# Performance work log

Measured on AMD Instinct MI355X. Metric: run time of the kernel, lower is better.

The kernel has to match this reference:

```python
import jax, jax.numpy as jnp
import numpy as np

B, P, C, F = 16, 1000, 91, 1024      # images, proposals/img, classes (incl bg), box-head dim
H, W = 800, 800                      # image shape (all images same size)
SCORE_THRESH = 0.05
NMS_THRESH = 0.5
DETS = 100                           # detections_per_img
MIN_SIZE = 1e-2
BBOX_XFORM_CLIP = float(np.log(1000.0 / 16.0))
OFF = float(max(H, W) + 2)           # class offset unit for batched (class-aware) NMS


def setup_inputs() -> dict:
    key = jax.random.key(0)
    k1, k2, k3, k4 = jax.random.split(key, 4)
    box_features = jax.random.normal(k1, (B * P, F), jnp.float32)
    Wc = jax.random.normal(k2, (F, C), jnp.float32) * 0.02
    bc = jnp.zeros((C,), jnp.float32)
    Wb = jax.random.normal(k3, (F, C * 4), jnp.float32) * 0.02
    bb = jnp.zeros((C * 4,), jnp.float32)
    u = jax.random.uniform(k4, (B, P, 4), jnp.float32)
    x1 = u[..., 0] * (W * 0.8)
    y1 = u[..., 1] * (H * 0.8)
    x2 = x1 + 16.0 + u[..., 2] * (W * 0.2)
    y2 = y1 + 16.0 + u[..., 3] * (H * 0.2)
    proposals = jnp.stack([x1, y1, x2, y2], axis=-1)
    return dict(box_features=box_features, Wc=Wc, bc=bc, Wb=Wb, bb=bb,
                proposals=proposals)


def _decode_and_clip(regs, props):
    # regs: [N, C, 4] deltas; props: [N, 4] xyxy. bbox_reg_weights = (1,1,1,1).
    w = props[:, 2] - props[:, 0]
    h = props[:, 3] - props[:, 1]
    cx = props[:, 0] + 0.5 * w
    cy = props[:, 1] + 0.5 * h
    dx, dy = regs[..., 0], regs[..., 1]
    dw = jnp.minimum(regs[..., 2], BBOX_XFORM_CLIP)
    dh = jnp.minimum(regs[..., 3], BBOX_XFORM_CLIP)
    pcx = dx * w[:, None] + cx[:, None]
    pcy = dy * h[:, None] + cy[:, None]
    pw = jnp.exp(dw) * w[:, None]
    ph = jnp.exp(dh) * h[:, None]
    x1 = jnp.clip(pcx - 0.5 * pw, 0.0, float(W))
    y1 = jnp.clip(pcy - 0.5 * ph, 0.0, float(H))
    x2 = jnp.clip(pcx + 0.5 * pw, 0.0, float(W))
    y2 = jnp.clip(pcy + 0.5 * ph, 0.0, float(H))
    return jnp.stack([x1, y1, x2, y2], axis=-1)  # [N, C, 4]


def _iou_one_vs_all(box, boxes):
    ix1 = jnp.maximum(box[0], boxes[:, 0])
    iy1 = jnp.maximum(box[1], boxes[:, 1])
    ix2 = jnp.minimum(box[2], boxes[:, 2])
    iy2 = jnp.minimum(box[3], boxes[:, 3])
    inter = jnp.clip(ix2 - ix1, 0.0) * jnp.clip(iy2 - iy1, 0.0)
    a1 = (box[2] - box[0]) * (box[3] - box[1])
    a2 = (boxes[:, 2] - boxes[:, 0]) * (boxes[:, 3] - boxes[:, 1])
    return inter / (a1 + a2 - inter + 1e-9)


def _greedy_nms(boxes, scores):
    # boxes: [M,4] (class-offset), scores: [M] (-inf = filtered out).
    # Returns selected indices [DETS] and scores [DETS] (0 where no valid pick).
    def body(i, st):
        sc, sel, ss = st
        j = jnp.argmax(sc)
        s = sc[j]
        iou = _iou_one_vs_all(boxes[j], boxes)
        sc = jnp.where(iou > NMS_THRESH, -jnp.inf, sc)  # suppresses j itself too
        valid = s > 0.0
        sel = sel.at[i].set(jnp.where(valid, j.astype(jnp.int32), 0))
        ss = ss.at[i].set(jnp.where(valid, s, 0.0))
        return sc, sel, ss
    init = (scores, jnp.zeros((DETS,), jnp.int32), jnp.zeros((DETS,), jnp.float32))
    _, sel, ss = jax.lax.fori_loop(0, DETS, body, init)
    return sel, ss


def reference(box_features, Wc, bc, Wb, bb, proposals):
    # Box predictor (FastRCNNPredictor-style linear heads).
    class_logits = box_features @ Wc + bc                  # [B*P, C]
    box_regression = (box_features @ Wb + bb).reshape(-1, C, 4)
    # Decode per-class boxes against proposals, clip to image.
    pred = _decode_and_clip(box_regression, proposals.reshape(-1, 4))  # [B*P, C, 4]
    scores = jax.nn.softmax(class_logits, axis=-1)         # [B*P, C]
    # Drop background class 0; flatten (proposal, class) per image.
    M = P * (C - 1)
    boxes_all = pred[:, 1:, :].reshape(B, M, 4)
    scores_all = scores[:, 1:].reshape(B, M)
    labels_all = jnp.tile(jnp.arange(1, C, dtype=jnp.int32), P)  # [M]
    # Score threshold + remove tiny boxes (mask instead of dynamic filter).
    bw = boxes_all[..., 2] - boxes_all[..., 0]
    bh = boxes_all[..., 3] - boxes_all[..., 1]
    keep = (scores_all > SCORE_THRESH) & (bw >= MIN_SIZE) & (bh >= MIN_SIZE)
    scores_m = jnp.where(keep, scores_all, -jnp.inf)
    # Class-aware batched NMS via per-class coordinate offsets.
    boxes_off = boxes_all + (labels_all.astype(jnp.float32) * OFF)[None, :, None]
    sel, det_scores = jax.vmap(_greedy_nms)(boxes_off, scores_m)   # [B,DETS]
    det_boxes = jnp.take_along_axis(boxes_all, sel[..., None], axis=1)  # [B,DETS,4]
    det_labels = labels_all[sel]                                        # [B,DETS]
    valid = det_scores > 0.0
    det_boxes = det_boxes * valid[..., None]
    det_labels = jnp.where(valid, det_labels, 0)
    return det_boxes, det_scores, det_labels
```

## Files before the change

### kernel.cpp

```cpp
#include <hip/hip_runtime.h>
#include <hip/hip_bf16.h>
#include <math.h>

typedef unsigned long long ull;
typedef __attribute__((ext_vector_type(8))) short bf16x8;
typedef __attribute__((ext_vector_type(4))) float f32x4;

#define BB_ 16
#define PP_ 1000
#define CC_ 91
#define FF_ 1024
#define DETS_ 100
#define CAP_ 2048
#define CAND_MAX (BB_ * CAP_)
#define SURV_CAP 2048
#define CLS_CAP 256
#define BLK_CAND 720
#define IMG_W 800.0f
#define IMG_H 800.0f
#define OFF_ 802.0f
#define SCORE_TH 0.05f
#define PRE_TH 0.0494f
#define NMS_TH 0.5f
#define MIN_SZ 0.01f
#define BBOX_CLIP_D 4.135166556742356

__device__ __forceinline__ ushort bf16_hi(float v) {
    return (ushort)((__float_as_uint(v) + 0x8000u) >> 16);
}

__global__ __launch_bounds__(256) void prep_weights(
    const float* __restrict__ Wb, float* __restrict__ Wbt,
    const float* __restrict__ Wc, ushort* __restrict__ Wcth,
    ushort* __restrict__ Wctl)
{
    const int idx = blockIdx.x * 256 + threadIdx.x;
    if (idx < CC_ * 4 * FF_) {
        const int c = idx >> 12;
        const int j = (idx >> 10) & 3;
        const int k = idx & 1023;
        Wbt[idx] = (c < 1) ? 0.f : Wb[(size_t)k * (CC_ * 4) + 4 * c + j];
    }
    if (idx < 96 * FF_) {
        const int c = idx >> 10, k = idx & 1023;
        const float v = (c < CC_) ? Wc[(size_t)k * CC_ + c] : 0.f;
        const ushort h = bf16_hi(v);
        const float hf = __uint_as_float(((unsigned)h) << 16);
        Wcth[idx] = h;
        Wctl[idx] = bf16_hi(v - hf);
    }
}

__global__ __launch_bounds__(256) void prepass_mfma(
    const float* __restrict__ A, const ushort* __restrict__ Wcth,
    const ushort* __restrict__ Wctl, const float* __restrict__ bc,
    int* __restrict__ rowlist, int* __restrict__ nrowsp)
{
    __shared__ union __align__(16) SM {
        struct { ushort Ah[32][40]; ushort Al[32][40];
                 ushort Bh[96][40]; ushort Bl[96][40]; } t;
        float Ssc[32][97];
    } sm;

    const int tid = threadIdx.x;
    const int row0 = blockIdx.x * 32;
    const int lane = tid & 63;
    const int w = tid >> 6;
    const int rowOff = (w & 1) * 16;
    const int colOff = (w >> 1) * 48;

    const int arow = tid >> 3;
    const int ak4 = (tid & 7) * 4;
    const int bcol = tid >> 1;
    const int bkh = (tid & 1) * 16;

    f32x4 acc0 = {0.f, 0.f, 0.f, 0.f};
    f32x4 acc1 = {0.f, 0.f, 0.f, 0.f};
    f32x4 acc2 = {0.f, 0.f, 0.f, 0.f};

    float4 avP = *(const float4*)(A + (size_t)(row0 + arow) * FF_ + ak4);
    uint4 bhP0 = make_uint4(0,0,0,0), bhP1 = make_uint4(0,0,0,0);
    uint4 blP0 = make_uint4(0,0,0,0), blP1 = make_uint4(0,0,0,0);
    if (tid < 192) {
        const ushort* sh = Wcth + (size_t)bcol * FF_ + bkh;
        const ushort* sl = Wctl + (size_t)bcol * FF_ + bkh;
        bhP0 = *(const uint4*)(sh);  bhP1 = *(const uint4*)(sh + 8);
        blP0 = *(const uint4*)(sl);  blP1 = *(const uint4*)(sl + 8);
    }

    for (int k0 = 0; k0 < FF_; k0 += 32) {
        {
            float vv[4] = {avP.x, avP.y, avP.z, avP.w};
            ushort hh[4], ll[4];
#pragma unroll
            for (int j = 0; j < 4; ++j) {
                hh[j] = bf16_hi(vv[j]);
                const float hf = __uint_as_float(((unsigned)hh[j]) << 16);
                ll[j] = bf16_hi(vv[j] - hf);
            }
            *(uint2*)&sm.t.Ah[arow][ak4] = make_uint2(
                (unsigned)hh[0] | ((unsigned)hh[1] << 16),
                (unsigned)hh[2] | ((unsigned)hh[3] << 16));
            *(uint2*)&sm.t.Al[arow][ak4] = make_uint2(
                (unsigned)ll[0] | ((unsigned)ll[1] << 16),
                (unsigned)ll[2] | ((unsigned)ll[3] << 16));
        }
        if (tid < 192) {
            *(uint4*)&sm.t.Bh[bcol][bkh]     = bhP0;
            *(uint4*)&sm.t.Bh[bcol][bkh + 8] = bhP1;
            *(uint4*)&sm.t.Bl[bcol][bkh]     = blP0;
            *(uint4*)&sm.t.Bl[bcol][bkh + 8] = blP1;
        }

        const int kn = k0 + 32;
        if (kn < FF_) {
            avP = *(const float4*)(A + (size_t)(row0 + arow) * FF_ + kn + ak4);
            if (tid < 192) {
                const ushort* sh = Wcth + (size_t)bcol * FF_ + kn + bkh;
                const ushort* sl = Wctl + (size_t)bcol * FF_ + kn + bkh;
                bhP0 = *(const uint4*)(sh);  bhP1 = *(const uint4*)(sh + 8);
                blP0 = *(const uint4*)(sl);  blP1 = *(const uint4*)(sl + 8);
            }
        }
        __syncthreads();

        const int ar = rowOff + (lane & 15);
        const int ke = (lane >> 4) * 8;
        const bf16x8 aH = *(const bf16x8*)&sm.t.Ah[ar][ke];
        const bf16x8 aL = *(const bf16x8*)&sm.t.Al[ar][ke];
#pragma unroll
        for (int ct = 0; ct < 3; ++ct) {
            const int bc_ = colOff + ct * 16 + (lane & 15);
            const bf16x8 bH = *(const bf16x8*)&sm.t.Bh[bc_][ke];
            const bf16x8 bL = *(const bf16x8*)&sm.t.Bl[bc_][ke];
            f32x4* acc = (ct == 0) ? &acc0 : (ct == 1) ? &acc1 : &acc2;
            *acc = __builtin_amdgcn_mfma_f32_16x16x32_bf16(aH, bH, *acc, 0, 0, 0);
            *acc = __builtin_amdgcn_mfma_f32_16x16x32_bf16(aH, bL, *acc, 0, 0, 0);
            *acc = __builtin_amdgcn_mfma_f32_16x16x32_bf16(aL, bH, *acc, 0, 0, 0);
        }
        __syncthreads();
    }

    {
        const int r0 = rowOff + (lane >> 4) * 4;
        const int cb = colOff + (lane & 15);
#pragma unroll
        for (int reg = 0; reg < 4; ++reg) {
            const int row = r0 + reg;
            int c = cb;
            if (c < CC_) sm.Ssc[row][c] = acc0[reg] + bc[c];
            c = cb + 16;
            if (c < CC_) sm.Ssc[row][c] = acc1[reg] + bc[c];
            c = cb + 32;
            if (c < CC_) sm.Ssc[row][c] = acc2[reg] + bc[c];
        }
    }
    __syncthreads();

    if (tid < 32) {
        float m_all = sm.Ssc[tid][0];
        float m_fg = -INFINITY;
        for (int c = 1; c < CC_; ++c) {
            const float lv = sm.Ssc[tid][c];
            m_all = fmaxf(m_all, lv);
            m_fg = fmaxf(m_fg, lv);
        }
        float denom = 0.f;
        for (int c = 0; c < CC_; ++c) denom += expf(sm.Ssc[tid][c] - m_all);
        const float maxsc = expf(m_fg - m_all) / denom;
        if (maxsc > PRE_TH) {
            const int pos = atomicAdd(nrowsp, 1);
            rowlist[pos] = row0 + tid;
        }
    }
}

template<bool USE_T>
__global__ __launch_bounds__(512) void logits_fp64_rows(
    const float* __restrict__ A, const float* __restrict__ Wc,
    const float* __restrict__ bc,
    const float* __restrict__ Wb, const float* __restrict__ Wbt,
    const float* __restrict__ bb, const float* __restrict__ props,
    const int* __restrict__ rowlist, const int* __restrict__ nrowsp,
    float* __restrict__ cs, int* __restrict__ clab,
    int* __restrict__ corig, int* __restrict__ cpidx,
    int* __restrict__ cnt,
    float* __restrict__ cx1, float* __restrict__ cy1,
    float* __restrict__ cx2, float* __restrict__ cy2)
{
    const int nr = *nrowsp;
    const int row0 = blockIdx.x * 8;
    if (row0 >= nr) return;

    __shared__ union __align__(16) SM {
        struct { float Af[2][32][12]; float Bs[2][32][98]; } t;
        struct { int cp[BLK_CAND]; int cc[BLK_CAND]; int cg[BLK_CAND]; } d;
    } sm;
    __shared__ __align__(16) double dcomb[256][3];
    __shared__ float Ssc[8][97];
    __shared__ int ncand;

    const int tid = threadIdx.x;
    const int kg = tid >> 8;
    const int l = tid & 255;
    const int kbase = kg * 512;
    const int r = l >> 5;
    const int c0 = (l & 31) * 3;

    if (tid == 0) ncand = 0;

    const int aslot = l >> 3;
    const int akq = (l & 7) * 4;
    const float* Arow = nullptr;
    if (l < 64) {
        const int ridx = min(row0 + aslot, nr - 1);
        Arow = A + (size_t)rowlist[ridx] * FF_ + kbase;
    }
    const int bk = l >> 3;
    const int bn = (l & 7) * 12;

    double acc[3] = {0.0, 0.0, 0.0};

    float4 avP = make_float4(0.f, 0.f, 0.f, 0.f);
    if (l < 64) avP = *reinterpret_cast<const float4*>(Arow + akq);
    float bvP[12];
#pragma unroll
    for (int jj = 0; jj < 12; ++jj) {
        const int c = bn + jj;
        bvP[jj] = (c < CC_) ? Wc[(size_t)(kbase + bk) * CC_ + c] : 0.f;
    }

    for (int k0 = 0; k0 < 512; k0 += 32) {
        if (l < 64) {
            sm.t.Af[kg][akq + 0][aslot] = avP.x;
            sm.t.Af[kg][akq + 1][aslot] = avP.y;
            sm.t.Af[kg][akq + 2][aslot] = avP.z;
            sm.t.Af[kg][akq + 3][aslot] = avP.w;
        }
#pragma unroll
        for (int jj = 0; jj < 12; ++jj) sm.t.Bs[kg][bk][bn + jj] = bvP[jj];

        const int kn = k0 + 32;
        if (kn < 512) {
            if (l < 64)
                avP = *reinterpret_cast<const float4*>(Arow + kn + akq);
#pragma unroll
            for (int jj = 0; jj < 12; ++jj) {
                const int c = bn + jj;
                bvP[jj] = (c < CC_) ? Wc[(size_t)(kbase + kn + bk) * CC_ + c] : 0.f;
            }
        }
        __syncthreads();

#pragma unroll
        for (int k = 0; k < 32; ++k) {
            const double a0 = (double)sm.t.Af[kg][k][r];
            const double b0 = (double)sm.t.Bs[kg][k][c0 + 0];
            const double b1 = (double)sm.t.Bs[kg][k][c0 + 1];
            const double b2 = (double)sm.t.Bs[kg][k][c0 + 2];
            acc[0] += a0 * b0;
            acc[1] += a0 * b1;
            acc[2] += a0 * b2;
        }
        __syncthreads();
    }

    if (kg == 1) {
#pragma unroll
        for (int j = 0; j < 3; ++j) dcomb[l][j] = acc[j];
    }
    __syncthreads();
    if (kg == 0) {
#pragma unroll
        for (int j = 0; j < 3; ++j) {
            const int c = c0 + j;
            if (c < CC_) {
                const double v = acc[j] + dcomb[l][j];
                Ssc[r][c] = __fadd_rn((float)v, bc[c]);
            }
        }
    }
    __syncthreads();

    {
        const int w = tid >> 6;
        const int lane = tid & 63;
        if (w < 8 && row0 + w < nr) {
            const int p = rowlist[row0 + w];
            const int b = p / PP_;
            const int pi = p - b * PP_;

            const float l1 = Ssc[w][lane];
            const float l2 = (lane < CC_ - 64) ? Ssc[w][lane + 64] : -INFINITY;
            float m = fmaxf(l1, l2);
#pragma unroll
            for (int off = 32; off > 0; off >>= 1)
                m = fmaxf(m, __shfl_xor(m, off));

            double d = exp((double)l1 - (double)m);
            if (lane < CC_ - 64) d += exp((double)l2 - (double)m);
#pragma unroll
            for (int off = 1; off < 64; off <<= 1)
                d += __shfl_xor(d, off);

#pragma unroll
            for (int q = 0; q < 2; ++q) {
                const int c = lane + q * 64;
                if (c >= 1 && c < CC_) {
                    const double sd = exp((double)Ssc[w][c] - (double)m) / d;
                    const float score = (float)sd;
                    if (score > SCORE_TH) {
                        const int pos = atomicAdd(&cnt[b], 1);
                        if (pos < CAP_) {
                            const int g = b * CAP_ + pos;
                            cs[g] = score;
                            clab[g] = c;
                            corig[g] = pi * (CC_ - 1) + (c - 1);
                            cpidx[g] = p;
                            const int slot = atomicAdd(&ncand, 1);
                            if (slot < BLK_CAND) {
                                sm.d.cp[slot] = p;
                                sm.d.cc[slot] = c;
                                sm.d.cg[slot] = g;
                            }
                        }
                    }
                }
            }
        }
    }
    __syncthreads();

    {
        const int w = tid >> 6;
        const int lane = tid & 63;
        const int nc = min(ncand, BLK_CAND);
        for (int ci = w; ci < nc; ci += 8) {
            const int p = sm.d.cp[ci];
            const int c = sm.d.cc[ci];
            const int g = sm.d.cg[ci];

            const float* fr = A + (size_t)p * FF_;
            double a0 = 0.0, a1 = 0.0, a2 = 0.0, a3 = 0.0;
            if (USE_T) {
                const float* w0 = Wbt + (size_t)c * 4096;
                for (int k = lane; k < FF_; k += 64) {
                    const double f = (double)fr[k];
                    a0 += f * (double)w0[k];
                    a1 += f * (double)w0[1024 + k];
                    a2 += f * (double)w0[2048 + k];
                    a3 += f * (double)w0[3072 + k];
                }
            } else {
                const float* wb0 = Wb + 4 * c;
                for (int k = lane; k < FF_; k += 64) {
                    const double f = (double)fr[k];
                    const float4 wv = *reinterpret_cast<const float4*>(
                        wb0 + (size_t)k * (CC_ * 4));
                    a0 += f * (double)wv.x; a1 += f * (double)wv.y;
                    a2 += f * (double)wv.z; a3 += f * (double)wv.w;
                }
            }
#pragma unroll
            for (int off = 32; off > 0; off >>= 1) {
                a0 += __shfl_xor(a0, off);
                a1 += __shfl_xor(a1, off);
                a2 += __shfl_xor(a2, off);
                a3 += __shfl_xor(a3, off);
            }

            if (lane == 0) {
                const float dx = __fadd_rn((float)a0, bb[4 * c + 0]);
                const float dy = __fadd_rn((float)a1, bb[4 * c + 1]);
                const float clipf = (float)BBOX_CLIP_D;
                const float dw = fminf(__fadd_rn((float)a2, bb[4 * c + 2]), clipf);
                const float dh = fminf(__fadd_rn((float)a3, bb[4 * c + 3]), clipf);

                const float px1 = props[(size_t)p * 4 + 0];
                const float py1 = props[(size_t)p * 4 + 1];
                const float px2 = props[(size_t)p * 4 + 2];
                const float py2 = props[(size_t)p * 4 + 3];
                const float wq = __fsub_rn(px2, px1);
                const float hq = __fsub_rn(py2, py1);
                const float cxq = __fadd_rn(px1, __fmul_rn(0.5f, wq));
                const float cyq = __fadd_rn(py1, __fmul_rn(0.5f, hq));

                const float pcx = __fadd_rn(__fmul_rn(dx, wq), cxq);
                const float pcy = __fadd_rn(__fmul_rn(dy, hq), cyq);
                const float ew = (float)exp((double)dw);
                const float eh = (float)exp((double)dh);
                const float pw = __fmul_rn(ew, wq);
                const float ph = __fmul_rn(eh, hq);

                const float hw = __fmul_rn(0.5f, pw);
                const float hh = __fmul_rn(0.5f, ph);
                const float bx1 = fminf(fmaxf(__fsub_rn(pcx, hw), 0.f), IMG_W);
                const float by1 = fminf(fmaxf(__fsub_rn(pcy, hh), 0.f), IMG_H);
                const float bx2 = fminf(fmaxf(__fadd_rn(pcx, hw), 0.f), IMG_W);
                const float by2 = fminf(fmaxf(__fadd_rn(pcy, hh), 0.f), IMG_H);

                cx1[g] = bx1; cy1[g] = by1; cx2[g] = bx2; cy2[g] = by2;
                if (!(__fsub_rn(bx2, bx1) >= MIN_SZ && __fsub_rn(by2, by1) >= MIN_SZ)) {
                    cs[g] = -INFINITY;
                }
            }
        }
    }
}

__global__ __launch_bounds__(64) void nms_class(
    const float* __restrict__ c_x1, const float* __restrict__ c_y1,
    const float* __restrict__ c_x2, const float* __restrict__ c_y2,
    const float* __restrict__ c_s, const int* __restrict__ c_lab,
    const int* __restrict__ c_orig, const int* __restrict__ cnt,
    ull* __restrict__ skey, float* __restrict__ sx1v, float* __restrict__ sy1v,
    float* __restrict__ sx2v, float* __restrict__ sy2v,
    int* __restrict__ slabv, int* __restrict__ scnt)
{
    const int blk = blockIdx.x;
    const int b = blk / (CC_ - 1);
    const int c = 1 + (blk - b * (CC_ - 1));
    const int lane = threadIdx.x;

    __shared__ ull kk[CLS_CAP];
    __shared__ float x1s[CLS_CAP], y1s[CLS_CAP], x2s[CLS_CAP], y2s[CLS_CAP];

    const int n = min(cnt[b], CAP_);

    int mcnt = 0;
    for (int i0 = 0; i0 < n; i0 += 64) {
        const int i = i0 + lane;
        bool take = false;
        float s = 0.f; int so = 0; int g = 0;
        if (i < n) {
            g = b * CAP_ + i;
            if (c_lab[g] == c) {
                s = c_s[g];
                if (s > 0.f) { take = true; so = c_orig[g]; }
            }
        }
        const ull bal = __ballot(take);
        if (take) {
            const int pos = mcnt + __popcll(bal & ((1ull << lane) - 1ull));
            if (pos < CLS_CAP) {
                kk[pos] = ((ull)__float_as_uint(s) << 32) |
                          (unsigned int)(0x7FFFFFFF - so);
                x1s[pos] = c_x1[g]; y1s[pos] = c_y1[g];
                x2s[pos] = c_x2[g]; y2s[pos] = c_y2[g];
            }
        }
        mcnt += (int)__popcll(bal);
    }
    mcnt = min(mcnt, CLS_CAP);
    if (mcnt == 0) return;
    __syncthreads();

    while (true) {
        ull best = 0ull;
        for (int i = lane; i < mcnt; i += 64) best = (kk[i] > best) ? kk[i] : best;
#pragma unroll
        for (int off = 32; off > 0; off >>= 1) {
            const ull o = __shfl_xor(best, off);
            best = (o > best) ? o : best;
        }
        if (best == 0ull) break;

        int wsl = -1;
        for (int i = lane; i < mcnt; i += 64) if (kk[i] == best) wsl = i;
        const ull bal = __ballot(wsl >= 0);
        const int wlane = (int)__ffsll((long long)bal) - 1;
        wsl = __shfl(wsl, wlane);

        const float wx1 = x1s[wsl], wy1 = y1s[wsl];
        const float wx2 = x2s[wsl], wy2 = y2s[wsl];

        if (lane == 0) {
            const int sp = atomicAdd(&scnt[b], 1);
            if (sp < SURV_CAP) {
                const int sg = b * SURV_CAP + sp;
                skey[sg] = best;
                sx1v[sg] = wx1; sy1v[sg] = wy1;
                sx2v[sg] = wx2; sy2v[sg] = wy2;
                slabv[sg] = c;
            }
        }

        const float off = __fmul_rn((float)c, OFF_);
        const float ax1 = __fadd_rn(wx1, off), ay1 = __fadd_rn(wy1, off);
        const float ax2 = __fadd_rn(wx2, off), ay2 = __fadd_rn(wy2, off);
        const float a1 = __fmul_rn(__fsub_rn(ax2, ax1), __fsub_rn(ay2, ay1));
        for (int i = lane; i < mcnt; i += 64) {
            if (kk[i] == 0ull) continue;
            const float bx1 = __fadd_rn(x1s[i], off), by1 = __fadd_rn(y1s[i], off);
            const float bx2 = __fadd_rn(x2s[i], off), by2 = __fadd_rn(y2s[i], off);
            const float ix1 = fmaxf(ax1, bx1), iy1 = fmaxf(ay1, by1);
            const float ix2 = fminf(ax2, bx2), iy2 = fminf(ay2, by2);
            const float inter = __fmul_rn(fmaxf(__fsub_rn(ix2, ix1), 0.f),
                                          fmaxf(__fsub_rn(iy2, iy1), 0.f));
            const float a2 = __fmul_rn(__fsub_rn(bx2, bx1), __fsub_rn(by2, by1));
            const float den = __fadd_rn(__fsub_rn(__fadd_rn(a1, a2), inter), 1e-9f);
            const float iou = __fdiv_rn(inter, den);
            if (iou > NMS_TH) kk[i] = 0ull;
        }
        __syncthreads();
    }
}

__global__ __launch_bounds__(256) void nms_merge(
    const ull* __restrict__ skey, const float* __restrict__ sx1v,
    const float* __restrict__ sy1v, const float* __restrict__ sx2v,
    const float* __restrict__ sy2v, const int* __restrict__ slabv,
    const int* __restrict__ scnt, float* __restrict__ out)
{
    const int b = blockIdx.x;
    const int t = threadIdx.x;

    __shared__ ull k_[SURV_CAP];
    __shared__ int id_[SURV_CAP];

    const int m = min(scnt[b], SURV_CAP);
    int N2 = 128;
    while (N2 < m) N2 <<= 1;

    for (int i = t; i < N2; i += 256) {
        k_[i] = (i < m) ? skey[b * SURV_CAP + i] : 0ull;
        id_[i] = i;
    }
    __syncthreads();

    for (int ksz = 2; ksz <= N2; ksz <<= 1) {
        for (int j = ksz >> 1; j > 0; j >>= 1) {
            for (int i = t; i < N2; i += 256) {
                const int ixj = i ^ j;
                if (ixj > i) {
                    const ull a = k_[i], cc = k_[ixj];
                    const bool desc = ((i & ksz) == 0);
                    if (desc ? (a < cc) : (a > cc)) {
                        k_[i] = cc; k_[ixj] = a;
                        const int tmp = id_[i]; id_[i] = id_[ixj]; id_[ixj] = tmp;
                    }
                }
            }
            __syncthreads();
        }
    }

    const int boxes_base = 0;
    const int scores_base = BB_ * DETS_ * 4;
    const int labels_base = BB_ * DETS_ * 5;

    for (int r = t; r < DETS_; r += 256) {
        const ull key = (r < N2) ? k_[r] : 0ull;
        float* bo = out + boxes_base + (size_t)(b * DETS_ + r) * 4;
        if (key != 0ull) {
            const int sg = b * SURV_CAP + id_[r];
            bo[0] = sx1v[sg]; bo[1] = sy1v[sg];
            bo[2] = sx2v[sg]; bo[3] = sy2v[sg];
            out[scores_base + b * DETS_ + r] = __uint_as_float((unsigned)(key >> 32));
            out[labels_base + b * DETS_ + r] = (float)slabv[sg];
        } else {
            bo[0] = 0.f; bo[1] = 0.f; bo[2] = 0.f; bo[3] = 0.f;
            out[scores_base + b * DETS_ + r] = 0.f;
            out[labels_base + b * DETS_ + r] = 0.f;
        }
    }
}

extern "C" void kernel_launch(void* const* d_in, const int* in_sizes, int n_in,
                              void* d_out, int out_size, void* d_ws, size_t ws_size,
                              hipStream_t stream)
{
    const float* feat  = (const float*)d_in[0];
    const float* Wc    = (const float*)d_in[1];
    const float* bc    = (const float*)d_in[2];
    const float* Wb    = (const float*)d_in[3];
    const float* bb    = (const float*)d_in[4];
    const float* props = (const float*)d_in[5];
    for (int i = 0; i < n_in; ++i) {
        const float* q = (const float*)d_in[i];
        switch (in_sizes[i]) {
            case 16384000: feat  = q; break;
            case 93184:    Wc    = q; break;
            case 91:       bc    = q; break;
            case 372736:   Wb    = q; break;
            case 364:      bb    = q; break;
            case 64000:    props = q; break;
        }
    }
    float* out = (float*)d_out;

    char* ws = (char*)d_ws;
    int*   cnt    = (int*)ws;
    int*   scnt   = (int*)(ws + 64);
    int*   nrowsp = (int*)(ws + 128);
    float* cs    = (float*)(ws + 256);
    int*   clab  = (int*)(cs + CAND_MAX);
    int*   corig = clab + CAND_MAX;
    int*   cpidx = corig + CAND_MAX;
    float* cx1   = (float*)(cpidx + CAND_MAX);
    float* cy1   = cx1 + CAND_MAX;
    float* cx2   = cy1 + CAND_MAX;
    float* cy2   = cx2 + CAND_MAX;
    ull*   skey  = (ull*)(cy2 + CAND_MAX);
    float* sx1v  = (float*)(skey + (size_t)BB_ * SURV_CAP);
    float* sy1v  = sx1v + (size_t)BB_ * SURV_CAP;
    float* sx2v  = sy1v + (size_t)BB_ * SURV_CAP;
    float* sy2v  = sx2v + (size_t)BB_ * SURV_CAP;
    int*   slabv = (int*)(sy2v + (size_t)BB_ * SURV_CAP);
    int*   rowlist = slabv + (size_t)BB_ * SURV_CAP;
    ushort* Wcth = (ushort*)(rowlist + 16384);
    ushort* Wctl = Wcth + 96 * FF_;
    float* Wbt   = (float*)(Wctl + 96 * FF_);

    const size_t need = ((char*)(Wbt + CC_ * 4 * FF_)) - ws;
    const bool useT = (ws_size >= need);

    hipMemsetAsync(ws, 0, 256, stream);

    prep_weights<<<(CC_ * 4 * FF_ + 255) / 256, 256, 0, stream>>>(
        Wb, Wbt, Wc, Wcth, Wctl);

    prepass_mfma<<<BB_ * PP_ / 32, 256, 0, stream>>>(feat, Wcth, Wctl, bc,
        rowlist, nrowsp);

    if (useT)
        logits_fp64_rows<true><<<BB_ * PP_ / 8, 512, 0, stream>>>(
            feat, Wc, bc, Wb, Wbt, bb, props, rowlist, nrowsp,
            cs, clab, corig, cpidx, cnt, cx1, cy1, cx2, cy2);
    else
        logits_fp64_rows<false><<<BB_ * PP_ / 8, 512, 0, stream>>>(
            feat, Wc, bc, Wb, Wbt, bb, props, rowlist, nrowsp,
            cs, clab, corig, cpidx, cnt, cx1, cy1, cx2, cy2);

    nms_class<<<BB_ * (CC_ - 1), 64, 0, stream>>>(
        cx1, cy1, cx2, cy2, cs, clab, corig, cnt,
        skey, sx1v, sy1v, sx2v, sy2v, slabv, scnt);

    nms_merge<<<BB_, 256, 0, stream>>>(
        skey, sx1v, sy1v, sx2v, sy2v, slabv, scnt, out);
}
```

Before: 249.5 us.

## Compute fp64 class logits one row per wave and reuse staged feature rows

Replaces the shared-memory tiled fp64 GEMM, which split K across two halves, with a simpler scheme: each wave copies one feature row into LDS and computes two class columns per lane, reading Wc straight from global memory. The staged feature row is then reused for the box-regression dot products instead of being fetched again from global memory. This removes the tile syncs and the cross-half reduction, but Wc is now read separately by every wave with no shared tile reuse, and shared memory grows to 32KB for the rows.

```diff
diff --git a/kernel.cpp b/kernel.cpp
--- a/kernel.cpp
+++ b/kernel.cpp
@@ -192,137 +192,86 @@
     const int row0 = blockIdx.x * 8;
     if (row0 >= nr) return;
 
-    __shared__ union __align__(16) SM {
-        struct { float Af[2][32][12]; float Bs[2][32][98]; } t;
-        struct { int cp[BLK_CAND]; int cc[BLK_CAND]; int cg[BLK_CAND]; } d;
-    } sm;
-    __shared__ __align__(16) double dcomb[256][3];
-    __shared__ float Ssc[8][97];
+    __shared__ __align__(16) float Arow[8][1024];
+    __shared__ float Ssc[8][92];
+    __shared__ int cp[BLK_CAND], ccl[BLK_CAND], cg[BLK_CAND], crw[BLK_CAND];
     __shared__ int ncand;
 
     const int tid = threadIdx.x;
-    const int kg = tid >> 8;
-    const int l = tid & 255;
-    const int kbase = kg * 512;
-    const int r = l >> 5;
-    const int c0 = (l & 31) * 3;
+    const int w = tid >> 6;
+    const int lane = tid & 63;
+    const bool rowok = (row0 + w < nr);
 
     if (tid == 0) ncand = 0;
-
-    const int aslot = l >> 3;
-    const int akq = (l & 7) * 4;
-    const float* Arow = nullptr;
-    if (l < 64) {
-        const int ridx = min(row0 + aslot, nr - 1);
-        Arow = A + (size_t)rowlist[ridx] * FF_ + kbase;
-    }
-    const int bk = l >> 3;
-    const int bn = (l & 7) * 12;
-
-    double acc[3] = {0.0, 0.0, 0.0};
-
-    float4 avP = make_float4(0.f, 0.f, 0.f, 0.f);
-    if (l < 64) avP = *reinterpret_cast<const float4*>(Arow + akq);
-    float bvP[12];
-#pragma unroll
-    for (int jj = 0; jj < 12; ++jj) {
-        const int c = bn + jj;
-        bvP[jj] = (c < CC_) ? Wc[(size_t)(kbase + bk) * CC_ + c] : 0.f;
-    }
-
-    for (int k0 = 0; k0 < 512; k0 += 32) {
-        if (l < 64) {
-            sm.t.Af[kg][akq + 0][aslot] = avP.x;
-            sm.t.Af[kg][akq + 1][aslot] = avP.y;
-            sm.t.Af[kg][akq + 2][aslot] = avP.z;
-            sm.t.Af[kg][akq + 3][aslot] = avP.w;
-        }
-#pragma unroll
-        for (int jj = 0; jj < 12; ++jj) sm.t.Bs[kg][bk][bn + jj] = bvP[jj];
-
-        const int kn = k0 + 32;
-        if (kn < 512) {
-            if (l < 64)
-                avP = *reinterpret_cast<const float4*>(Arow + kn + akq);
-#pragma unroll
-            for (int jj = 0; jj < 12; ++jj) {
-                const int c = bn + jj;
-                bvP[jj] = (c < CC_) ? Wc[(size_t)(kbase + kn + bk) * CC_ + c] : 0.f;
-            }
-        }
-        __syncthreads();
-
-#pragma unroll
-        for (int k = 0; k < 32; ++k) {
-            const double a0 = (double)sm.t.Af[kg][k][r];
-            const double b0 = (double)sm.t.Bs[kg][k][c0 + 0];
-            const double b1 = (double)sm.t.Bs[kg][k][c0 + 1];
-            const double b2 = (double)sm.t.Bs[kg][k][c0 + 2];
-            acc[0] += a0 * b0;
-            acc[1] += a0 * b1;
-            acc[2] += a0 * b2;
-        }
-        __syncthreads();
-    }
-
-    if (kg == 1) {
-#pragma unroll
-        for (int j = 0; j < 3; ++j) dcomb[l][j] = acc[j];
-    }
     __syncthreads();
-    if (kg == 0) {
-#pragma unroll
-        for (int j = 0; j < 3; ++j) {
-            const int c = c0 + j;
-            if (c < CC_) {
-                const double v = acc[j] + dcomb[l][j];
-                Ssc[r][c] = __fadd_rn((float)v, bc[c]);
-            }
-        }
-    }
-    __syncthreads();
-
-    {
-        const int w = tid >> 6;
-        const int lane = tid & 63;
-        if (w < 8 && row0 + w < nr) {
-            const int p = rowlist[row0 + w];
-            const int b = p / PP_;
-            const int pi = p - b * PP_;
-
-            const float l1 = Ssc[w][lane];
-            const float l2 = (lane < CC_ - 64) ? Ssc[w][lane + 64] : -INFINITY;
-            float m = fmaxf(l1, l2);
-#pragma unroll
-            for (int off = 32; off > 0; off >>= 1)
-                m = fmaxf(m, __shfl_xor(m, off));
-
-            double d = exp((double)l1 - (double)m);
-            if (lane < CC_ - 64) d += exp((double)l2 - (double)m);
-#pragma unroll
-            for (int off = 1; off < 64; off <<= 1)
-                d += __shfl_xor(d, off);
-
-#pragma unroll
-            for (int q = 0; q < 2; ++q) {
-                const int c = lane + q * 64;
-                if (c >= 1 && c < CC_) {
-                    const double sd = exp((double)Ssc[w][c] - (double)m) / d;
-                    const float score = (float)sd;
-                    if (score > SCORE_TH) {
-                        const int pos = atomicAdd(&cnt[b], 1);
-                        if (pos < CAP_) {
-                            const int g = b * CAP_ + pos;
-                            cs[g] = score;
-                            clab[g] = c;
-                            corig[g] = pi * (CC_ - 1) + (c - 1);
-                            cpidx[g] = p;
-                            const int slot = atomicAdd(&ncand, 1);
-                            if (slot < BLK_CAND) {
-                                sm.d.cp[slot] = p;
-                                sm.d.cc[slot] = c;
-                                sm.d.cg[slot] = g;
-                            }
+
+    int p = 0, b = 0, pi = 0;
+    if (rowok) {
+        p = rowlist[row0 + w];
+        b = p / PP_;
+        pi = p - b * PP_;
+        const float* gA = A + (size_t)p * FF_;
+#pragma unroll
+        for (int j = 0; j < 4; ++j) {
+            const int off = j * 256 + lane * 4;
+            *(float4*)&Arow[w][off] = *(const float4*)(gA + off);
+        }
+
+        const int c1 = lane;
+        const int c2 = lane + 64;
+        double acc0 = 0.0, acc1 = 0.0;
+        if (c2 < CC_) {
+#pragma unroll 8
+            for (int k = 0; k < FF_; ++k) {
+                const double a = (double)Arow[w][k];
+                acc0 += a * (double)Wc[(size_t)k * CC_ + c1];
+                acc1 += a * (double)Wc[(size_t)k * CC_ + c2];
+            }
+        } else {
+#pragma unroll 8
+            for (int k = 0; k < FF_; ++k) {
+                const double a = (double)Arow[w][k];
+                acc0 += a * (double)Wc[(size_t)k * CC_ + c1];
+            }
+        }
+        Ssc[w][c1] = __fadd_rn((float)acc0, bc[c1]);
+        if (c2 < CC_) Ssc[w][c2] = __fadd_rn((float)acc1, bc[c2]);
+    }
+
+    if (rowok) {
+        const float l1 = Ssc[w][lane];
+        const float l2 = (lane < CC_ - 64) ? Ssc[w][lane + 64] : -INFINITY;
+        float m = fmaxf(l1, l2);
+#pragma unroll
+        for (int off = 32; off > 0; off >>= 1)
+            m = fmaxf(m, __shfl_xor(m, off));
+
+        double d = exp((double)l1 - (double)m);
+        if (lane < CC_ - 64) d += exp((double)l2 - (double)m);
+#pragma unroll
+        for (int off = 1; off < 64; off <<= 1)
+            d += __shfl_xor(d, off);
+
+#pragma unroll
+        for (int q = 0; q < 2; ++q) {
+            const int c = lane + q * 64;
+            if (c >= 1 && c < CC_) {
+                const double sd = exp((double)Ssc[w][c] - (double)m) / d;
+                const float score = (float)sd;
+                if (score > SCORE_TH) {
+                    const int pos = atomicAdd(&cnt[b], 1);
+                    if (pos < CAP_) {
+                        const int g = b * CAP_ + pos;
+                        cs[g] = score;
+                        clab[g] = c;
+                        corig[g] = pi * (CC_ - 1) + (c - 1);
+                        cpidx[g] = p;
+                        const int slot = atomicAdd(&ncand, 1);
+                        if (slot < BLK_CAND) {
+                            cp[slot] = p;
+                            ccl[slot] = c;
+                            cg[slot] = g;
+                            crw[slot] = w;
                         }
                     }
                 }
@@ -332,15 +281,13 @@
     __syncthreads();
 
     {
-        const int w = tid >> 6;
-        const int lane = tid & 63;
         const int nc = min(ncand, BLK_CAND);
         for (int ci = w; ci < nc; ci += 8) {
-            const int p = sm.d.cp[ci];
-            const int c = sm.d.cc[ci];
-            const int g = sm.d.cg[ci];
-
-            const float* fr = A + (size_t)p * FF_;
+            const int pc = cp[ci];
+            const int c = ccl[ci];
+            const int g = cg[ci];
+            const float* fr = &Arow[crw[ci]][0];
+
             double a0 = 0.0, a1 = 0.0, a2 = 0.0, a3 = 0.0;
             if (USE_T) {
                 const float* w0 = Wbt + (size_t)c * 4096;
@@ -376,10 +323,10 @@
                 const float dw = fminf(__fadd_rn((float)a2, bb[4 * c + 2]), clipf);
                 const float dh = fminf(__fadd_rn((float)a3, bb[4 * c + 3]), clipf);
 
-                const float px1 = props[(size_t)p * 4 + 0];
-                const float py1 = props[(size_t)p * 4 + 1];
-                const float px2 = props[(size_t)p * 4 + 2];
-                const float py2 = props[(size_t)p * 4 + 3];
+                const float px1 = props[(size_t)pc * 4 + 0];
+                const float py1 = props[(size_t)pc * 4 + 1];
+                const float px2 = props[(size_t)pc * 4 + 2];
+                const float py2 = props[(size_t)pc * 4 + 3];
                 const float wq = __fsub_rn(px2, px1);
                 const float hq = __fsub_rn(py2, py1);
                 const float cxq = __fadd_rn(px1, __fmul_rn(0.5f, wq));
```

After: 310.7 us. 24.6% more time.
